# Kernel optimization log

Measured on AMD Instinct MI355X. Metric: run time of the kernel, lower is better.

The kernel has to match this reference:

```python
import jax, jax.numpy as jnp
import numpy as np

HEADS = 4
F_OUT = 64
NEG_SLOPE = 0.2


def setup_inputs() -> dict:
    key = jax.random.key(0)
    k1, k2, k3, k4 = jax.random.split(key, 4)
    N, F_IN = 4096, 256
    x = jax.random.normal(k1, (N, F_IN), dtype=jnp.float32)
    adj = jax.random.randint(k2, (N, N), 0, 2, dtype=jnp.int32)
    # nn.Linear stores weight [out, in]; we store transposed [in, out] for x @ W
    W = jax.random.normal(k3, (F_IN, F_OUT * HEADS), dtype=jnp.float32) * (1.0 / np.sqrt(F_IN))
    a = jax.random.normal(k4, (2 * F_OUT, 1), dtype=jnp.float32) * 0.1
    return {"x": x, "adj": adj, "W": W, "a": a}


def reference(x, adj, W, a):
    N = x.shape[0]
    h = (x @ W).reshape(N, HEADS, F_OUT)              # [N, H, F]
    # matmul(cat(h_i, h_j), a) == h_i @ a1 + h_j @ a2 (exact, avoids O(N^2*2F) h_cat)
    a1 = a[:F_OUT, 0]
    a2 = a[F_OUT:, 0]
    e_i = jnp.einsum('nhf,f->nh', h, a1)              # [N, H]
    e_j = jnp.einsum('nhf,f->nh', h, a2)              # [N, H]
    e = e_i[:, None, :] + e_j[None, :, :]             # [N, N, H]
    e = jnp.where(e > 0, e, NEG_SLOPE * e)            # LeakyReLU(0.2)
    e = jnp.where(adj[:, :, None] == 0, -jnp.inf, e)
    attention = jax.nn.softmax(e, axis=1)             # softmax over source nodes j
    h_prime = jnp.einsum('ijh,jhf->ihf', attention, h)  # [N, H, F]
    return h_prime.mean(axis=1)                       # heads > 1 -> mean over heads
```

## Files before the change

kernel.cpp:

```cpp
#include <hip/hip_runtime.h>

#define N     4096
#define FIN   256
#define CC    256
#define HEADS 4
#define FOUT  64
#define XPITCH 266

typedef __attribute__((ext_vector_type(8))) short bf16x8;
typedef __attribute__((ext_vector_type(4))) float f32x4;

__device__ inline short f2bf(float f) {
    unsigned u = __builtin_bit_cast(unsigned, f);
    unsigned r = u + 0x7fffu + ((u >> 16) & 1u);
    return (short)(r >> 16);
}

__global__ __launch_bounds__(256) void gat_k1a(const float* __restrict__ x,
                                               const float* __restrict__ W,
                                               const float* __restrict__ a,
                                               short* __restrict__ hF,
                                               float2* __restrict__ e1f,
                                               float2* __restrict__ e2f,
                                               float* __restrict__ out) {
    __shared__ __align__(16) short xs[64][XPITCH];
    __shared__ __align__(16) short wts[64][XPITCH];
    __shared__ __align__(16) short hbuf[64][74];
    const int t    = threadIdx.x;
    const int bid  = blockIdx.x;
    const int lane = t & 63;
    const int w    = t >> 6;

    ((float4*)out)[bid * 256 + t] = make_float4(0.f, 0.f, 0.f, 0.f);

    const int hd = bid >> 6;
    const int n0 = (bid & 63) * 64;
    const int c0 = hd * 64;

    {
        const float4* xsrc = (const float4*)(x + (size_t)n0 * FIN);
        #pragma unroll
        for (int it = 0; it < 16; ++it) {
            const int fi = it * 256 + t;
            const float4 v = xsrc[fi];
            short4 o;
            o.x = f2bf(v.x); o.y = f2bf(v.y); o.z = f2bf(v.z); o.w = f2bf(v.w);
            *(short4*)&xs[fi >> 6][(fi & 63) * 4] = o;
        }
    }
    {
        const int c  = t & 63;
        const int k4 = (t >> 6) * 4;
        #pragma unroll
        for (int it = 0; it < 16; ++it) {
            const int k = it * 16 + k4;
            short4 pk;
            pk.x = f2bf(W[(k + 0) * CC + c0 + c]);
            pk.y = f2bf(W[(k + 1) * CC + c0 + c]);
            pk.z = f2bf(W[(k + 2) * CC + c0 + c]);
            pk.w = f2bf(W[(k + 3) * CC + c0 + c]);
            *(short4*)&wts[c][k] = pk;
        }
    }
    __syncthreads();

    const int m = lane & 15;
    const int q = lane >> 4;

    f32x4 acc[4];
    #pragma unroll
    for (int ct = 0; ct < 4; ++ct) acc[ct] = (f32x4){0.f, 0.f, 0.f, 0.f};

    #pragma unroll
    for (int ks = 0; ks < 8; ++ks) {
        const bf16x8 af = *(const bf16x8*)&xs[w * 16 + m][ks * 32 + q * 8];
        #pragma unroll
        for (int ct = 0; ct < 4; ++ct) {
            const bf16x8 bf_ = *(const bf16x8*)&wts[ct * 16 + m][ks * 32 + q * 8];
            acc[ct] = __builtin_amdgcn_mfma_f32_16x16x32_bf16(af, bf_, acc[ct], 0, 0, 0);
        }
    }

    const float a1v[4] = {a[m], a[16 + m], a[32 + m], a[48 + m]};
    const float a2v[4] = {a[64 + m], a[80 + m], a[96 + m], a[112 + m]};
    #pragma unroll
    for (int r = 0; r < 4; ++r) {
        float s1 = 0.f, s2 = 0.f;
        #pragma unroll
        for (int ct = 0; ct < 4; ++ct) {
            s1 = fmaf(acc[ct][r], a1v[ct], s1);
            s2 = fmaf(acc[ct][r], a2v[ct], s2);
        }
        #pragma unroll
        for (int sh = 1; sh < 16; sh <<= 1) {
            s1 += __shfl_xor(s1, sh, 64);
            s2 += __shfl_xor(s2, sh, 64);
        }
        if (m == 0) {
            const int n = n0 + w * 16 + q * 4 + r;
            e1f[(size_t)hd * N + n] = make_float2(__expf(s1), __expf(0.2f * s1));
            e2f[(size_t)hd * N + n] = make_float2(__expf(s2), __expf(0.2f * s2));
        }
    }

    #pragma unroll
    for (int ct = 0; ct < 4; ++ct)
        #pragma unroll
        for (int r = 0; r < 4; ++r)
            hbuf[ct * 16 + m][w * 16 + q * 4 + r] = f2bf(acc[ct][r]);
    __syncthreads();

    {
        const int lp = t & 63;
        const int ft = t >> 6;
        const int mm = lp & 15;
        const int qq = lp >> 4;
        #pragma unroll
        for (int c2 = 0; c2 < 2; ++c2) {
            const bf16x8 hv = *(const bf16x8*)&hbuf[ft * 16 + mm][c2 * 32 + qq * 8];
            const size_t jc = (size_t)(n0 >> 5) + c2;
            *(bf16x8*)(hF + ((((size_t)hd * 128 + jc) * 4 + ft) * 64 + lp) * 8) = hv;
        }
    }
}

__global__ __launch_bounds__(256) void gat_k1b(const int* __restrict__ adj,
                                               unsigned* __restrict__ adjb) {
    const int t    = threadIdx.x;
    const int lane = t & 63;
    const int w    = t >> 6;
    const int row  = blockIdx.x * 2 + (w >> 1);
    const int half = w & 1;
    const int4* arow4 = (const int4*)(adj + (size_t)row * N) + half * 512;
    unsigned*   drow  = adjb + (size_t)row * 128 + half * 64;

    int4 ca[8];
    #pragma unroll
    for (int k = 0; k < 8; ++k)
        ca[k] = arow4[k * 64 + lane];
    #pragma unroll
    for (int k = 0; k < 8; ++k) {
        const int4 v = ca[k];
        unsigned n = (v.x != 0 ? 1u : 0u) | (v.y != 0 ? 2u : 0u) |
                     (v.z != 0 ? 4u : 0u) | (v.w != 0 ? 8u : 0u);
        unsigned b  = n   | ((unsigned)__shfl_xor((int)n,   1, 64) << 4);
        unsigned hw = b   | ((unsigned)__shfl_xor((int)b,   2, 64) << 8);
        unsigned d  = hw  | ((unsigned)__shfl_xor((int)hw,  4, 64) << 16);
        if ((lane & 7) == 0) drow[k * 8 + (lane >> 3)] = d;
    }
}

__global__ __launch_bounds__(512) void gat_k2a(const float2* __restrict__ e1f,
                                               const float2* __restrict__ e2f,
                                               const unsigned* __restrict__ adjb,
                                               float* __restrict__ Zg) {
    __shared__ __align__(16) float e2s[2 * N];
    const int t    = threadIdx.x;
    const int lane = t & 63;
    const int g    = t >> 6;
    const int bid  = blockIdx.x;
    const int hd   = bid >> 9;
    const int row  = (bid & 511) * 8 + g;

    {
        const float4* s = (const float4*)(e2f + (size_t)hd * N);
        float4* d = (float4*)e2s;
        #pragma unroll
        for (int r = 0; r < 4; ++r) d[t + r * 512] = s[t + r * 512];
    }
    __syncthreads();

    const float2 E1 = e1f[(size_t)hd * N + row];
    const unsigned* ar = adjb + (size_t)row * 128;
    float z = 0.f;
    #pragma unroll 4
    for (int k = 0; k < 64; ++k) {
        const int j = k * 64 + lane;
        const float2 p = ((const float2*)e2s)[j];
        const unsigned bd  = ar[(unsigned)j >> 5];
        const unsigned msk = 0u - ((bd >> (lane & 31)) & 1u);
        float wv = fmaxf(E1.x * p.x, E1.y * p.y);
        wv = __builtin_bit_cast(float, __builtin_bit_cast(unsigned, wv) & msk);
        z += wv;
    }
    #pragma unroll
    for (int sh = 1; sh < 64; sh <<= 1) z += __shfl_xor(z, sh, 64);
    if (lane == 0) Zg[(size_t)hd * N + row] = z;
}

__global__ __launch_bounds__(512, 4) void gat_k2b(const short* __restrict__ hF,
                                                  const unsigned* __restrict__ adjb,
                                                  const float2* __restrict__ e1f,
                                                  const float2* __restrict__ e2f,
                                                  const float* __restrict__ Zg,
                                                  float* __restrict__ out) {
    __shared__ __align__(16) short    hstage[2][4096];
    __shared__ __align__(16) float    e2s[2048];
    __shared__ __align__(16) unsigned adjl[128 * 36];
    const int t    = threadIdx.x;
    const int lane = t & 63;
    const int g    = t >> 6;
    const int bid  = blockIdx.x;
    const int xcd  = bid & 7;
    const int idx  = bid >> 3;
    const int hd   = idx & 3;
    const int jc   = (idx >> 2) & 3;
    const int it   = xcd | ((idx >> 4) << 3);
    const int i0   = it * 128;
    const int j0   = jc * 1024;
    const int m    = lane & 15;
    const int q    = lane >> 4;

    ((float4*)e2s)[t] = ((const float4*)(e2f + (size_t)hd * N + j0))[t];
    {
        const int row = t >> 2, part = t & 3;
        const uint4* src = (const uint4*)(adjb + (size_t)(i0 + row) * 128 + jc * 32 + part * 8);
        uint4* dst = (uint4*)(adjl + row * 36 + part * 8);
        dst[0] = src[0];
        dst[1] = src[1];
    }
    const uint4* gsrc = (const uint4*)(hF + ((size_t)hd * 128 + jc * 32) * 2048);
    ((uint4*)hstage[0])[t] = gsrc[t];
    __syncthreads();

    const int   rowi = i0 + g * 16 + m;
    const float2 E1r = e1f[(size_t)hd * N + rowi];
    const float  zs  = 0.25f / Zg[(size_t)hd * N + rowi];
    const float  E1x = E1r.x * zs;
    const float  E1y = E1r.y * zs;

    f32x4 acc[4];
    #pragma unroll
    for (int ft = 0; ft < 4; ++ft) acc[ft] = (f32x4){0.f, 0.f, 0.f, 0.f};

    const unsigned char* ab = ((const unsigned char*)adjl) + (g * 16 + m) * 144 + q;

    int cur = 0;
    #pragma unroll 2
    for (int mac = 0; mac < 16; ++mac) {
        const uint4 v = gsrc[(size_t)((mac + 1) & 15) * 512 + t];

        const short* hb = &hstage[cur][0];
        #pragma unroll
        for (int s = 0; s < 2; ++s) {
            const int jloc = mac * 64 + s * 32 + q * 8;
            const bf16x8 b0 = *(const bf16x8*)(hb + s * 2048 + 0 * 512 + lane * 8);
            const bf16x8 b1 = *(const bf16x8*)(hb + s * 2048 + 1 * 512 + lane * 8);
            const bf16x8 b2 = *(const bf16x8*)(hb + s * 2048 + 2 * 512 + lane * 8);
            const bf16x8 b3 = *(const bf16x8*)(hb + s * 2048 + 3 * 512 + lane * 8);
            const float4* ev = (const float4*)&e2s[2 * jloc];
            const float4 d0 = ev[0], d1 = ev[1], d2 = ev[2], d3 = ev[3];
            const unsigned bits = (unsigned)ab[(mac * 2 + s) * 4];

            const float ep[8] = {d0.x, d0.z, d1.x, d1.z, d2.x, d2.z, d3.x, d3.z};
            const float en[8] = {d0.y, d0.w, d1.y, d1.w, d2.y, d2.w, d3.y, d3.w};

            bf16x8 af;
            #pragma unroll
            for (int jj = 0; jj < 8; ++jj) {
                const unsigned msk = (unsigned)(((int)(bits << (31 - jj))) >> 31);
                float wv = fmaxf(E1x * ep[jj], E1y * en[jj]);
                wv = __builtin_bit_cast(float, __builtin_bit_cast(unsigned, wv) & msk);
                af[jj] = f2bf(wv);
            }

            acc[0] = __builtin_amdgcn_mfma_f32_16x16x32_bf16(af, b0, acc[0], 0, 0, 0);
            acc[1] = __builtin_amdgcn_mfma_f32_16x16x32_bf16(af, b1, acc[1], 0, 0, 0);
            acc[2] = __builtin_amdgcn_mfma_f32_16x16x32_bf16(af, b2, acc[2], 0, 0, 0);
            acc[3] = __builtin_amdgcn_mfma_f32_16x16x32_bf16(af, b3, acc[3], 0, 0, 0);
        }

        if (mac < 15) {
            ((uint4*)hstage[cur ^ 1])[t] = v;
            __syncthreads();
            cur ^= 1;
        }
    }

    #pragma unroll
    for (int ft = 0; ft < 4; ++ft)
        #pragma unroll
        for (int r = 0; r < 4; ++r)
            atomicAdd(&out[(size_t)(i0 + g * 16 + q * 4 + r) * FOUT + ft * 16 + m],
                      acc[ft][r]);
}

extern "C" void kernel_launch(void* const* d_in, const int* in_sizes, int n_in,
                              void* d_out, int out_size, void* d_ws, size_t ws_size,
                              hipStream_t stream) {
    const float* x   = (const float*)d_in[0];
    const int*   adj = (const int*)d_in[1];
    const float* W   = (const float*)d_in[2];
    const float* a   = (const float*)d_in[3];
    float* out = (float*)d_out;

    short*    hF   = (short*)d_ws;
    float2*   e1f  = (float2*)(hF + (size_t)HEADS * FOUT * N);
    float2*   e2f  = e1f + (size_t)HEADS * N;
    unsigned* adjb = (unsigned*)(e2f + (size_t)HEADS * N);
    float*    Zg   = (float*)(adjb + (size_t)N * 128);

    gat_k1a<<<256, 256, 0, stream>>>(x, W, a, hF, e1f, e2f, out);
    gat_k1b<<<2048, 256, 0, stream>>>(adj, adjb);
    gat_k2a<<<2048, 512, 0, stream>>>(e1f, e2f, adjb, Zg);
    gat_k2b<<<512, 512, 0, stream>>>(hF, adjb, e1f, e2f, Zg, out);
}
```

Before: 155.5 us.

## Fuse softmax denominator into attention kernel and replace atomics with split reduction

Removes the separate normalizer kernel by accumulating the softmax denominator alongside the weighted sum inside the main MFMA kernel. Each head/column-chunk slice now writes unnormalized partial numerators and denominators to workspace instead of doing atomicAdd into the output. A new small kernel sums the slices, divides by the denominator and averages over heads. The projection kernel moves to 512 threads, with half the waves idle during the MFMA, and no longer zeroes the output. The cost is an extra 16x N x 64 float workspace written and re-read, plus one more launch.

```diff
diff --git a/kernel.cpp b/kernel.cpp
--- a/kernel.cpp
+++ b/kernel.cpp
@@ -16,13 +16,12 @@
     return (short)(r >> 16);
 }
 
-__global__ __launch_bounds__(256) void gat_k1a(const float* __restrict__ x,
+__global__ __launch_bounds__(512) void gat_k1a(const float* __restrict__ x,
                                                const float* __restrict__ W,
                                                const float* __restrict__ a,
                                                short* __restrict__ hF,
                                                float2* __restrict__ e1f,
-                                               float2* __restrict__ e2f,
-                                               float* __restrict__ out) {
+                                               float2* __restrict__ e2f) {
     __shared__ __align__(16) short xs[64][XPITCH];
     __shared__ __align__(16) short wts[64][XPITCH];
     __shared__ __align__(16) short hbuf[64][74];
@@ -31,8 +30,6 @@
     const int lane = t & 63;
     const int w    = t >> 6;
 
-    ((float4*)out)[bid * 256 + t] = make_float4(0.f, 0.f, 0.f, 0.f);
-
     const int hd = bid >> 6;
     const int n0 = (bid & 63) * 64;
     const int c0 = hd * 64;
@@ -40,8 +37,8 @@
     {
         const float4* xsrc = (const float4*)(x + (size_t)n0 * FIN);
         #pragma unroll
-        for (int it = 0; it < 16; ++it) {
-            const int fi = it * 256 + t;
+        for (int it = 0; it < 8; ++it) {
+            const int fi = it * 512 + t;
             const float4 v = xsrc[fi];
             short4 o;
             o.x = f2bf(v.x); o.y = f2bf(v.y); o.z = f2bf(v.z); o.w = f2bf(v.w);
@@ -52,8 +49,8 @@
         const int c  = t & 63;
         const int k4 = (t >> 6) * 4;
         #pragma unroll
-        for (int it = 0; it < 16; ++it) {
-            const int k = it * 16 + k4;
+        for (int it = 0; it < 8; ++it) {
+            const int k = it * 32 + k4;
             short4 pk;
             pk.x = f2bf(W[(k + 0) * CC + c0 + c]);
             pk.y = f2bf(W[(k + 1) * CC + c0 + c]);
@@ -67,60 +64,60 @@
     const int m = lane & 15;
     const int q = lane >> 4;
 
-    f32x4 acc[4];
-    #pragma unroll
-    for (int ct = 0; ct < 4; ++ct) acc[ct] = (f32x4){0.f, 0.f, 0.f, 0.f};
-
-    #pragma unroll
-    for (int ks = 0; ks < 8; ++ks) {
-        const bf16x8 af = *(const bf16x8*)&xs[w * 16 + m][ks * 32 + q * 8];
-        #pragma unroll
-        for (int ct = 0; ct < 4; ++ct) {
-            const bf16x8 bf_ = *(const bf16x8*)&wts[ct * 16 + m][ks * 32 + q * 8];
-            acc[ct] = __builtin_amdgcn_mfma_f32_16x16x32_bf16(af, bf_, acc[ct], 0, 0, 0);
-        }
-    }
-
-    const float a1v[4] = {a[m], a[16 + m], a[32 + m], a[48 + m]};
-    const float a2v[4] = {a[64 + m], a[80 + m], a[96 + m], a[112 + m]};
-    #pragma unroll
-    for (int r = 0; r < 4; ++r) {
-        float s1 = 0.f, s2 = 0.f;
-        #pragma unroll
-        for (int ct = 0; ct < 4; ++ct) {
-            s1 = fmaf(acc[ct][r], a1v[ct], s1);
-            s2 = fmaf(acc[ct][r], a2v[ct], s2);
-        }
-        #pragma unroll
-        for (int sh = 1; sh < 16; sh <<= 1) {
-            s1 += __shfl_xor(s1, sh, 64);
-            s2 += __shfl_xor(s2, sh, 64);
-        }
-        if (m == 0) {
-            const int n = n0 + w * 16 + q * 4 + r;
-            e1f[(size_t)hd * N + n] = make_float2(__expf(s1), __expf(0.2f * s1));
-            e2f[(size_t)hd * N + n] = make_float2(__expf(s2), __expf(0.2f * s2));
-        }
-    }
-
-    #pragma unroll
-    for (int ct = 0; ct < 4; ++ct)
-        #pragma unroll
-        for (int r = 0; r < 4; ++r)
-            hbuf[ct * 16 + m][w * 16 + q * 4 + r] = f2bf(acc[ct][r]);
+    if (w < 4) {
+        f32x4 acc[4];
+        #pragma unroll
+        for (int ct = 0; ct < 4; ++ct) acc[ct] = (f32x4){0.f, 0.f, 0.f, 0.f};
+
+        #pragma unroll
+        for (int ks = 0; ks < 8; ++ks) {
+            const bf16x8 af = *(const bf16x8*)&xs[w * 16 + m][ks * 32 + q * 8];
+            #pragma unroll
+            for (int ct = 0; ct < 4; ++ct) {
+                const bf16x8 bf_ = *(const bf16x8*)&wts[ct * 16 + m][ks * 32 + q * 8];
+                acc[ct] = __builtin_amdgcn_mfma_f32_16x16x32_bf16(af, bf_, acc[ct], 0, 0, 0);
+            }
+        }
+
+        const float a1v[4] = {a[m], a[16 + m], a[32 + m], a[48 + m]};
+        const float a2v[4] = {a[64 + m], a[80 + m], a[96 + m], a[112 + m]};
+        #pragma unroll
+        for (int r = 0; r < 4; ++r) {
+            float s1 = 0.f, s2 = 0.f;
+            #pragma unroll
+            for (int ct = 0; ct < 4; ++ct) {
+                s1 = fmaf(acc[ct][r], a1v[ct], s1);
+                s2 = fmaf(acc[ct][r], a2v[ct], s2);
+            }
+            #pragma unroll
+            for (int sh = 1; sh < 16; sh <<= 1) {
+                s1 += __shfl_xor(s1, sh, 64);
+                s2 += __shfl_xor(s2, sh, 64);
+            }
+            if (m == 0) {
+                const int n = n0 + w * 16 + q * 4 + r;
+                e1f[(size_t)hd * N + n] = make_float2(__expf(s1), __expf(0.2f * s1));
+                e2f[(size_t)hd * N + n] = make_float2(__expf(s2), __expf(0.2f * s2));
+            }
+        }
+
+        #pragma unroll
+        for (int ct = 0; ct < 4; ++ct)
+            #pragma unroll
+            for (int r = 0; r < 4; ++r)
+                hbuf[ct * 16 + m][w * 16 + q * 4 + r] = f2bf(acc[ct][r]);
+    }
     __syncthreads();
 
     {
         const int lp = t & 63;
-        const int ft = t >> 6;
+        const int ft = (t >> 6) & 3;
+        const int c2 = t >> 8;
         const int mm = lp & 15;
         const int qq = lp >> 4;
-        #pragma unroll
-        for (int c2 = 0; c2 < 2; ++c2) {
-            const bf16x8 hv = *(const bf16x8*)&hbuf[ft * 16 + mm][c2 * 32 + qq * 8];
-            const size_t jc = (size_t)(n0 >> 5) + c2;
-            *(bf16x8*)(hF + ((((size_t)hd * 128 + jc) * 4 + ft) * 64 + lp) * 8) = hv;
-        }
+        const bf16x8 hv = *(const bf16x8*)&hbuf[ft * 16 + mm][c2 * 32 + qq * 8];
+        const size_t jc = (size_t)(n0 >> 5) + c2;
+        *(bf16x8*)(hF + ((((size_t)hd * 128 + jc) * 4 + ft) * 64 + lp) * 8) = hv;
     }
 }
 
@@ -150,50 +147,12 @@
     }
 }
 
-__global__ __launch_bounds__(512) void gat_k2a(const float2* __restrict__ e1f,
-                                               const float2* __restrict__ e2f,
-                                               const unsigned* __restrict__ adjb,
-                                               float* __restrict__ Zg) {
-    __shared__ __align__(16) float e2s[2 * N];
-    const int t    = threadIdx.x;
-    const int lane = t & 63;
-    const int g    = t >> 6;
-    const int bid  = blockIdx.x;
-    const int hd   = bid >> 9;
-    const int row  = (bid & 511) * 8 + g;
-
-    {
-        const float4* s = (const float4*)(e2f + (size_t)hd * N);
-        float4* d = (float4*)e2s;
-        #pragma unroll
-        for (int r = 0; r < 4; ++r) d[t + r * 512] = s[t + r * 512];
-    }
-    __syncthreads();
-
-    const float2 E1 = e1f[(size_t)hd * N + row];
-    const unsigned* ar = adjb + (size_t)row * 128;
-    float z = 0.f;
-    #pragma unroll 4
-    for (int k = 0; k < 64; ++k) {
-        const int j = k * 64 + lane;
-        const float2 p = ((const float2*)e2s)[j];
-        const unsigned bd  = ar[(unsigned)j >> 5];
-        const unsigned msk = 0u - ((bd >> (lane & 31)) & 1u);
-        float wv = fmaxf(E1.x * p.x, E1.y * p.y);
-        wv = __builtin_bit_cast(float, __builtin_bit_cast(unsigned, wv) & msk);
-        z += wv;
-    }
-    #pragma unroll
-    for (int sh = 1; sh < 64; sh <<= 1) z += __shfl_xor(z, sh, 64);
-    if (lane == 0) Zg[(size_t)hd * N + row] = z;
-}
-
 __global__ __launch_bounds__(512, 4) void gat_k2b(const short* __restrict__ hF,
                                                   const unsigned* __restrict__ adjb,
                                                   const float2* __restrict__ e1f,
                                                   const float2* __restrict__ e2f,
-                                                  const float* __restrict__ Zg,
-                                                  float* __restrict__ out) {
+                                                  float* __restrict__ num,
+                                                  float* __restrict__ Zp) {
     __shared__ __align__(16) short    hstage[2][4096];
     __shared__ __align__(16) float    e2s[2048];
     __shared__ __align__(16) unsigned adjl[128 * 36];
@@ -210,6 +169,7 @@
     const int j0   = jc * 1024;
     const int m    = lane & 15;
     const int q    = lane >> 4;
+    const int slice = hd * 4 + jc;
 
     ((float4*)e2s)[t] = ((const float4*)(e2f + (size_t)hd * N + j0))[t];
     {
@@ -223,15 +183,15 @@
     ((uint4*)hstage[0])[t] = gsrc[t];
     __syncthreads();
 
-    const int   rowi = i0 + g * 16 + m;
-    const float2 E1r = e1f[(size_t)hd * N + rowi];
-    const float  zs  = 0.25f / Zg[(size_t)hd * N + rowi];
-    const float  E1x = E1r.x * zs;
-    const float  E1y = E1r.y * zs;
+    const int    rowi = i0 + g * 16 + m;
+    const float2 E1r  = e1f[(size_t)hd * N + rowi];
+    const float  E1x  = E1r.x;
+    const float  E1y  = E1r.y;
 
     f32x4 acc[4];
     #pragma unroll
     for (int ft = 0; ft < 4; ++ft) acc[ft] = (f32x4){0.f, 0.f, 0.f, 0.f};
+    float zacc = 0.f;
 
     const unsigned char* ab = ((const unsigned char*)adjl) + (g * 16 + m) * 144 + q;
 
@@ -261,6 +221,7 @@
                 const unsigned msk = (unsigned)(((int)(bits << (31 - jj))) >> 31);
                 float wv = fmaxf(E1x * ep[jj], E1y * en[jj]);
                 wv = __builtin_bit_cast(float, __builtin_bit_cast(unsigned, wv) & msk);
+                zacc += wv;
                 af[jj] = f2bf(wv);
             }
 
@@ -277,12 +238,44 @@
         }
     }
 
+    zacc += __shfl_xor(zacc, 16, 64);
+    zacc += __shfl_xor(zacc, 32, 64);
+    if (lane < 16)
+        Zp[(size_t)slice * N + i0 + g * 16 + lane] = zacc;
+
+    {
+        float* nrow = num + ((size_t)slice * N + i0 + g * 16) * FOUT;
+        #pragma unroll
+        for (int ft = 0; ft < 4; ++ft)
+            #pragma unroll
+            for (int r = 0; r < 4; ++r)
+                nrow[(q * 4 + r) * FOUT + ft * 16 + m] = acc[ft][r];
+    }
+}
+
+__global__ __launch_bounds__(256) void gat_k3(const float* __restrict__ num,
+                                              const float* __restrict__ Zp,
+                                              float* __restrict__ out) {
+    const int g4 = blockIdx.x * 256 + threadIdx.x;
+    const int i  = g4 >> 4;
+    const int fo = (g4 & 15) * 4;
+    float4 r = make_float4(0.f, 0.f, 0.f, 0.f);
     #pragma unroll
-    for (int ft = 0; ft < 4; ++ft)
-        #pragma unroll
-        for (int r = 0; r < 4; ++r)
-            atomicAdd(&out[(size_t)(i0 + g * 16 + q * 4 + r) * FOUT + ft * 16 + m],
-                      acc[ft][r]);
+    for (int hd = 0; hd < 4; ++hd) {
+        float4 s = make_float4(0.f, 0.f, 0.f, 0.f);
+        float  z = 0.f;
+        #pragma unroll
+        for (int jc = 0; jc < 4; ++jc) {
+            const int sl = hd * 4 + jc;
+            const float4 v = *(const float4*)(num + ((size_t)sl * N + i) * FOUT + fo);
+            s.x += v.x; s.y += v.y; s.z += v.z; s.w += v.w;
+            z += Zp[(size_t)sl * N + i];
+        }
+        const float inv = 1.f / z;
+        r.x += s.x * inv; r.y += s.y * inv; r.z += s.z * inv; r.w += s.w * inv;
+    }
+    r.x *= 0.25f; r.y *= 0.25f; r.z *= 0.25f; r.w *= 0.25f;
+    *(float4*)(out + (size_t)i * FOUT + fo) = r;
 }
 
 extern "C" void kernel_launch(void* const* d_in, const int* in_sizes, int n_in,
@@ -298,10 +291,11 @@
     float2*   e1f  = (float2*)(hF + (size_t)HEADS * FOUT * N);
     float2*   e2f  = e1f + (size_t)HEADS * N;
     unsigned* adjb = (unsigned*)(e2f + (size_t)HEADS * N);
-    float*    Zg   = (float*)(adjb + (size_t)N * 128);
-
-    gat_k1a<<<256, 256, 0, stream>>>(x, W, a, hF, e1f, e2f, out);
+    float*    num  = (float*)(adjb + (size_t)N * 128);
+    float*    Zp   = num + (size_t)16 * N * FOUT;
+
+    gat_k1a<<<256, 512, 0, stream>>>(x, W, a, hF, e1f, e2f);
     gat_k1b<<<2048, 256, 0, stream>>>(adj, adjb);
-    gat_k2a<<<2048, 512, 0, stream>>>(e1f, e2f, adjb, Zg);
-    gat_k2b<<<512, 512, 0, stream>>>(hF, adjb, e1f, e2f, Zg, out);
-}
+    gat_k2b<<<512, 512, 0, stream>>>(hF, adjb, e1f, e2f, num, Zp);
+    gat_k3<<<256, 256, 0, stream>>>(num, Zp, out);
+}
```

Result: faster. 136.0 us (-12.5%).
